# Optimization experiments

Hardware: AMD Instinct MI355X
Metric: run time of the kernel (lower is better)

Reference implementation:

```python
import jax, jax.numpy as jnp
import numpy as np

# ---- dimensions / config (match init_kwargs / RFM2DConfig defaults) ----
N = 128          # grid points per side
M = 128          # number of random features
B = 8            # batch of coefficient fields
H = 1.0 / (N - 1)
DT, ETA, STEPS = 0.03, 1e-4, 34          # heat-equation smoothing (eq. 3.14)
EPS, FVAL = 1e-9, 1.0
SP, SM, DSIG = 1.0 / 12.0, -1.0 / 3.0, 0.15  # sigma_gamma params (eq. 3.13)


def _dst1(x):
    """DST-I along last axis via odd-extension FFT (length 2*(n+1))."""
    n = x.shape[-1]
    z = jnp.zeros(x.shape[:-1] + (1,), x.dtype)
    y = jnp.concatenate([z, x, z, -jnp.flip(x, axis=-1)], axis=-1)
    return -jnp.fft.fft(y, axis=-1)[..., 1:n + 1].imag


def _dst2(x):
    y = _dst1(x)
    return jnp.swapaxes(_dst1(jnp.swapaxes(y, -1, -2)), -1, -2)


def _idst2(x):
    # inverse DST-I is DST-I / (2*(n+1)) per axis
    n1, n2 = x.shape[-1], x.shape[-2]
    return _dst2(x) / (4.0 * (n1 + 1) * (n2 + 1))


def _poisson_denom():
    n = N - 2
    k = np.arange(1, n + 1)
    lam = 2.0 - 2.0 * np.cos(np.pi * k / (n + 1))
    return jnp.asarray((lam[:, None] + lam[None, :]) / H ** 2, jnp.float32)

DENOM = _poisson_denom()  # (N-2, N-2)


def poisson_solve(rhs):
    """Solve -Lap u = rhs on (0,1)^2, homogeneous Dirichlet BC. rhs: (...,N,N)."""
    ri = rhs[..., 1:-1, 1:-1]
    ui = _idst2(_dst2(ri) / DENOM)
    pad = [(0, 0)] * (rhs.ndim - 2) + [(1, 1), (1, 1)]
    return jnp.pad(ui, pad)  # zero boundary


def lap_neumann(u):
    """5-point Laplacian with replicate (homogeneous Neumann) padding."""
    pad = [(0, 0)] * (u.ndim - 2) + [(1, 1), (1, 1)]
    up = jnp.pad(u, pad, mode='edge')
    return (up[..., 2:, 1:-1] + up[..., :-2, 1:-1]
            + up[..., 1:-1, 2:] + up[..., 1:-1, :-2] - 4.0 * u) / H ** 2


def grad_central(u):
    """Centered FD gradient, one-sided at boundaries. Returns (du/dx, du/dy)."""
    dudx = jnp.concatenate([(u[..., 1:2, :] - u[..., 0:1, :]) / H,
                            (u[..., 2:, :] - u[..., :-2, :]) / (2.0 * H),
                            (u[..., -1:, :] - u[..., -2:-1, :]) / H], axis=-2)
    dudy = jnp.concatenate([(u[..., :, 1:2] - u[..., :, 0:1]) / H,
                            (u[..., :, 2:] - u[..., :, :-2]) / (2.0 * H),
                            (u[..., :, -1:] - u[..., :, -2:-1]) / H], axis=-1)
    return dudx, dudy


def sigma_gamma(r):
    return (SP - SM) * jax.nn.sigmoid(r / DSIG) + SM


def smooth_coefficient(a):
    v = a
    for _ in range(STEPS):  # fixed small step count (34)
        v = v + DT * ETA * lap_neumann(v)
    return v


def setup_inputs() -> dict:
    key = jax.random.key(0)
    k1, k2, k3, k4 = jax.random.split(key, 4)
    # permeability field bounded away from 0 so log(a_eps) is well defined
    a = 1.0 + 2.0 * jax.random.uniform(k1, (B, N, N), dtype=jnp.float32)
    theta1 = jax.random.normal(k2, (M, N, N), dtype=jnp.float32)
    theta2 = jax.random.normal(k3, (M, N, N), dtype=jnp.float32)
    alpha = jax.random.normal(k4, (M,), dtype=jnp.float32)
    return {"a": a, "theta1": theta1, "theta2": theta2, "alpha": alpha}


def reference(a, theta1, theta2, alpha):
    # _prepare_a: heat-equation smoothing + grad(log a_eps)
    a_eps = smooth_coefficient(a)                       # (B,N,N)
    loga = jnp.log(jnp.maximum(a_eps, EPS))
    dlx, dly = grad_central(loga)                       # (B,N,N) each
    # predictor: -Lap p0 = f * sigma_gamma(theta1) / a_eps
    s1 = sigma_gamma(theta1)                            # (M,N,N)
    rhs0 = FVAL * s1[None] / a_eps[:, None]             # (B,M,N,N)
    p0 = poisson_solve(rhs0)
    # corrector: add grad(log a_eps) . grad(p0), modulated by sigma_gamma(theta2)
    g0x, g0y = grad_central(p0)
    s2 = sigma_gamma(theta2)
    rhs1 = rhs0 + (dlx[:, None] * g0x + dly[:, None] * g0y) * s2[None]
    phi = poisson_solve(rhs1)                           # (B,M,N,N) features
    # linear readout over features
    return jnp.einsum('m,bmxy->bxy', alpha, phi)
```

## Files before the change

kernel.cpp:

```cpp
#include <hip/hip_runtime.h>
#include <math.h>

#ifndef M_PI
#define M_PI 3.14159265358979323846
#endif

typedef unsigned short u16;
typedef __attribute__((ext_vector_type(8))) short bf16x8;
typedef __attribute__((ext_vector_type(4))) float f32x4;
typedef __attribute__((ext_vector_type(4), aligned(4))) float f32x4u;
typedef __attribute__((ext_vector_type(16))) float f32x16;

#define LDW 136
#define LDWF 132

__device__ __forceinline__ float sigma_gamma(float r) {
    float s = 1.0f / (1.0f + __expf(r * (-1.0f / 0.15f)));
    return 0.4166666666666667f * s - 0.3333333333333333f;
}

__device__ __forceinline__ void split1(float x, u16& h, u16& l) {
    unsigned u = __float_as_uint(x);
    unsigned hb = u & 0xffff0000u;
    h = (u16)(hb >> 16);
    float d = x - __uint_as_float(hb);
    unsigned ud = __float_as_uint(d);
    l = (u16)((ud + 0x7fffu + ((ud >> 16) & 1u)) >> 16);
}

__global__ __launch_bounds__(256) void k_prep(
    u16* __restrict__ Shi, u16* __restrict__ Slo,
    u16* __restrict__ Qhi, u16* __restrict__ Qlo,
    u16* __restrict__ QThi, u16* __restrict__ QTlo,
    float* __restrict__ DINV, float* __restrict__ G) {
    int id = blockIdx.x * 256 + threadIdx.x;
    if (id >= 16384) return;
    int r = id >> 7, c = id & 127;
    u16 h, l;
    float s = 0.f, di = 0.f;
    if (r < 126 && c < 126) {
        int prod = ((r + 1) * (c + 1)) % 254;
        s = (float)sin((double)prod * (M_PI / 127.0));
        double sr = sin((double)(r + 1) * (M_PI / 254.0));
        double sc = sin((double)(c + 1) * (M_PI / 254.0));
        di = (float)(16.0 / (64516.0 * 16129.0 * 4.0 * (sr * sr + sc * sc)));
    }
    split1(s, h, l); Shi[id] = h; Slo[id] = l;
    DINV[id] = di;
    double nc = (c == 0) ? sqrt(1.0 / 128.0) : sqrt(2.0 / 128.0);
    float q = (float)(nc * cos(M_PI * (double)c * (double)(2 * r + 1) / 256.0));
    split1(q, h, l); Qhi[id] = h; Qlo[id] = l;
    double nr = (r == 0) ? sqrt(1.0 / 128.0) : sqrt(2.0 / 128.0);
    float qt = (float)(nr * cos(M_PI * (double)r * (double)(2 * c + 1) / 256.0));
    split1(qt, h, l); QThi[id] = h; QTlo[id] = l;
    double lr = 2.0 * cos(M_PI * (double)r / 128.0) - 2.0;
    double lc = 2.0 * cos(M_PI * (double)c / 128.0) - 2.0;
    G[id] = (float)pow(1.0 + 0.03 * 1e-4 * 16129.0 * (lr + lc), 34.0);
}

__global__ __launch_bounds__(256) void k_sg(
    const float* __restrict__ th1, const float* __restrict__ th2,
    const float* __restrict__ alpha,
    float* __restrict__ SG1, float* __restrict__ SG2a) {
    int id = (blockIdx.x * 256 + threadIdx.x) * 4;
    int m = id >> 14;
    float al = alpha[m];
    f32x4 a = *(const f32x4*)(th1 + id);
    f32x4 b = *(const f32x4*)(th2 + id);
    f32x4 o1, o2;
#pragma unroll
    for (int j = 0; j < 4; ++j) {
        o1[j] = sigma_gamma(a[j]);
        o2[j] = al * sigma_gamma(b[j]);
    }
    *(f32x4*)(SG1 + id) = o1;
    *(f32x4*)(SG2a + id) = o2;
}

template <bool DOD, bool LAST>
__device__ __forceinline__ void mm_pass32(u16* Xhi, u16* Xlo, float* UF,
                                          const u16* WH, const u16* WL,
                                          const float* Dg, int rt, int ct,
                                          int l31, int hb) {
    const int colX = ct * 32 + l31;
    f32x4 dpre[4];
    if (DOD) {
#pragma unroll
        for (int g = 0; g < 4; ++g)
            dpre[g] = *(const f32x4*)(Dg + colX * 128 + rt * 32 + 8 * g + 4 * hb);
    }
    f32x16 acc;
#pragma unroll
    for (int i = 0; i < 16; ++i) acc[i] = 0.f;
    const u16* xh = Xhi + (rt * 32 + l31) * LDW + hb * 8;
    const u16* xl = Xlo + (rt * 32 + l31) * LDW + hb * 8;
    const u16* wh = WH + (ct * 32 + l31) * LDW + hb * 8;
    const u16* wl = WL + (ct * 32 + l31) * LDW + hb * 8;
#pragma unroll
    for (int s = 0; s < 8; ++s) {
        bf16x8 ah = *(const bf16x8*)(xh + s * 16);
        bf16x8 al = *(const bf16x8*)(xl + s * 16);
        bf16x8 bh = *(const bf16x8*)(wh + s * 16);
        bf16x8 bl = *(const bf16x8*)(wl + s * 16);
        acc = __builtin_amdgcn_mfma_f32_32x32x16_bf16(ah, bh, acc, 0, 0, 0);
        acc = __builtin_amdgcn_mfma_f32_32x32x16_bf16(al, bh, acc, 0, 0, 0);
        acc = __builtin_amdgcn_mfma_f32_32x32x16_bf16(ah, bl, acc, 0, 0, 0);
    }
    f32x4 o[4];
    uint2 uh[4], ul[4];
#pragma unroll
    for (int g = 0; g < 4; ++g) {
        float v0 = acc[4 * g], v1 = acc[4 * g + 1];
        float v2 = acc[4 * g + 2], v3 = acc[4 * g + 3];
        if (DOD) {
            v0 *= dpre[g][0]; v1 *= dpre[g][1];
            v2 *= dpre[g][2]; v3 *= dpre[g][3];
        }
        if (LAST) {
            o[g] = f32x4{v0, v1, v2, v3};
        } else {
            u16 h0, l0, h1, l1, h2, l2, h3, l3;
            split1(v0, h0, l0); split1(v1, h1, l1);
            split1(v2, h2, l2); split1(v3, h3, l3);
            uh[g].x = (unsigned)h0 | ((unsigned)h1 << 16);
            uh[g].y = (unsigned)h2 | ((unsigned)h3 << 16);
            ul[g].x = (unsigned)l0 | ((unsigned)l1 << 16);
            ul[g].y = (unsigned)l2 | ((unsigned)l3 << 16);
        }
    }
    __syncthreads();
#pragma unroll
    for (int g = 0; g < 4; ++g) {
        const int rbase = rt * 32 + 8 * g + 4 * hb;
        if (LAST) {
            *(f32x4*)(UF + colX * LDWF + rbase) = o[g];
        } else {
            *(uint2*)(Xhi + colX * LDW + rbase) = uh[g];
            *(uint2*)(Xlo + colX * LDW + rbase) = ul[g];
        }
    }
    __syncthreads();
}

template <int MODE>
__global__ __launch_bounds__(1024, 4) void k_mega(
    const u16* __restrict__ WHg, const u16* __restrict__ WLg,
    const u16* __restrict__ WHg2, const u16* __restrict__ WLg2,
    const float* __restrict__ Dmat,
    const float* __restrict__ src, const float* __restrict__ aux,
    const float* __restrict__ th2, const float* __restrict__ alpha,
    const float* __restrict__ dlxc, const float* __restrict__ dlyc,
    float* __restrict__ o1, float* __restrict__ o2, float* __restrict__ o3,
    float* __restrict__ o4) {
    __shared__ __align__(16) char SM[139264];
    u16* Xhi = (u16*)SM;
    u16* Xlo = (u16*)(SM + 34816);
    float* UF = (float*)SM;
    u16* WH = (u16*)(SM + 69632);
    u16* WL = (u16*)(SM + 104448);
    float* LG = (float*)(SM + 69632);

    const int tid = threadIdx.x;

    if (MODE == 0 && blockIdx.x >= 8) {
        float* red = (float*)SM;
        const int px0 = (blockIdx.x - 8) * 128;
        const int pl = tid & 127, mg = tid >> 7;
        float acc = 0.f;
        for (int i = 0; i < 16; ++i) {
            int m = mg * 16 + i;
            acc += alpha[m] * th2[m * 16384 + px0 + pl];
        }
        red[tid] = acc;
        __syncthreads();
        if (tid < 128) {
            float sum = 0.f;
#pragma unroll
            for (int g = 0; g < 8; ++g) sum += red[tid + g * 128];
            o4[px0 + tid] = sum;
        }
        return;
    }

    const int wave = tid >> 6, lane = tid & 63;
    const int rt = wave >> 2, ct = wave & 3;
    const int l31 = lane & 31, hb = lane >> 5;

    int b, m0;
    if (MODE == 1) { b = blockIdx.x >> 5; m0 = (blockIdx.x & 31) * 4; }
    else { b = blockIdx.x; m0 = 0; }

#pragma unroll
    for (int p = 0; p < 2; ++p) {
        int ch = tid + p * 1024;
        int r = ch >> 4, j0 = (ch & 15) * 8;
        *(uint4*)&WH[r * LDW + j0] = *(const uint4*)(WHg + r * 128 + j0);
        *(uint4*)&WL[r * LDW + j0] = *(const uint4*)(WLg + r * 128 + j0);
    }

    float tac[16];
    if (MODE == 1) {
#pragma unroll
        for (int i = 0; i < 16; ++i) tac[i] = 0.f;
    }

    const int ML = (MODE == 1) ? 4 : 1;
    for (int mi = 0; mi < ML; ++mi) {
#pragma unroll
        for (int p = 0; p < 2; ++p) {
            int ch = tid + p * 1024;
            int row = ch >> 4, c0 = (ch & 15) * 8;
            float v[8];
            if (MODE == 1) {
                const float* t1 = src + (size_t)(m0 + mi) * 16384;
                const float* iv = aux + b * 16384;
                if (row < 126) {
                    int base = (row + 1) * 128 + 1 + c0;
                    f32x4u ta = *(const f32x4u*)(t1 + base);
                    f32x4u tb = *(const f32x4u*)(t1 + base + 4);
                    f32x4u ia = *(const f32x4u*)(iv + base);
                    f32x4u ib = *(const f32x4u*)(iv + base + 4);
#pragma unroll
                    for (int j = 0; j < 8; ++j) {
                        float tv = (j < 4) ? ta[j] : tb[j - 4];
                        float ivv = (j < 4) ? ia[j] : ib[j - 4];
                        v[j] = (c0 + j < 126) ? tv * ivv : 0.f;
                    }
                } else {
#pragma unroll
                    for (int j = 0; j < 8; ++j) v[j] = 0.f;
                }
            } else {
                f32x4 p0 = *(const f32x4*)(src + b * 16384 + ch * 8);
                f32x4 p1 = *(const f32x4*)(src + b * 16384 + ch * 8 + 4);
#pragma unroll
                for (int j = 0; j < 4; ++j) { v[j] = p0[j]; v[j + 4] = p1[j]; }
            }
            unsigned hw[4], lw[4];
#pragma unroll
            for (int k = 0; k < 4; ++k) {
                u16 ha, la, hbb, lb;
                split1(v[2 * k], ha, la);
                split1(v[2 * k + 1], hbb, lb);
                hw[k] = (unsigned)ha | ((unsigned)hbb << 16);
                lw[k] = (unsigned)la | ((unsigned)lb << 16);
            }
            *(uint4*)&Xhi[row * LDW + c0] = make_uint4(hw[0], hw[1], hw[2], hw[3]);
            *(uint4*)&Xlo[row * LDW + c0] = make_uint4(lw[0], lw[1], lw[2], lw[3]);
        }
        __syncthreads();

        mm_pass32<false, false>(Xhi, Xlo, UF, WH, WL, nullptr, rt, ct, l31, hb);
        mm_pass32<true, false>(Xhi, Xlo, UF, WH, WL, Dmat, rt, ct, l31, hb);
        if (MODE == 0) {
#pragma unroll
            for (int p = 0; p < 2; ++p) {
                int ch = tid + p * 1024;
                int r = ch >> 4, j0 = (ch & 15) * 8;
                *(uint4*)&WH[r * LDW + j0] = *(const uint4*)(WHg2 + r * 128 + j0);
                *(uint4*)&WL[r * LDW + j0] = *(const uint4*)(WLg2 + r * 128 + j0);
            }
            __syncthreads();
        }
        mm_pass32<false, false>(Xhi, Xlo, UF, WH, WL, nullptr, rt, ct, l31, hb);
        mm_pass32<false, true>(Xhi, Xlo, UF, WH, WL, nullptr, rt, ct, l31, hb);

        if (MODE == 0) {
#pragma unroll
            for (int p = 0; p < 2; ++p) {
                int ch = tid + p * 1024;
                int row = ch >> 4, c0 = (ch & 15) * 8;
                f32x4 a0 = *(const f32x4*)(UF + row * LDWF + c0);
                f32x4 a1 = *(const f32x4*)(UF + row * LDWF + c0 + 4);
                f32x4 i0, i1, g0, g1;
#pragma unroll
                for (int j = 0; j < 4; ++j) {
                    i0[j] = 1.0f / a0[j]; i1[j] = 1.0f / a1[j];
                    g0[j] = logf(fmaxf(a0[j], 1e-9f));
                    g1[j] = logf(fmaxf(a1[j], 1e-9f));
                }
                *(f32x4*)(o1 + b * 16384 + ch * 8) = i0;
                *(f32x4*)(o1 + b * 16384 + ch * 8 + 4) = i1;
                *(f32x4*)(LG + row * LDWF + c0) = g0;
                *(f32x4*)(LG + row * LDWF + c0 + 4) = g1;
            }
            __syncthreads();
#pragma unroll
            for (int p = 0; p < 2; ++p) {
                int ch = tid + p * 1024;
                int i = ch >> 4, c0 = (ch & 15) * 8;
                if (i < 1 || i > 126) continue;
                f32x4 up0 = *(const f32x4*)(LG + (i + 1) * LDWF + c0);
                f32x4 up1 = *(const f32x4*)(LG + (i + 1) * LDWF + c0 + 4);
                f32x4 um0 = *(const f32x4*)(LG + (i - 1) * LDWF + c0);
                f32x4 um1 = *(const f32x4*)(LG + (i - 1) * LDWF + c0 + 4);
                float win[13];
                win[0] = (c0 > 0) ? LG[i * LDWF + c0 - 1] : 0.f;
                f32x4 va = *(const f32x4*)(LG + i * LDWF + c0);
                f32x4 vb = *(const f32x4*)(LG + i * LDWF + c0 + 4);
                f32x4 vc = *(const f32x4*)(LG + i * LDWF + c0 + 8);
#pragma unroll
                for (int j = 0; j < 4; ++j) {
                    win[1 + j] = va[j]; win[5 + j] = vb[j]; win[9 + j] = vc[j];
                }
#pragma unroll
                for (int e = 0; e < 8; ++e) {
                    int j = c0 + e;
                    if (j < 1 || j > 126) continue;
                    float upv = (e < 4) ? up0[e] : up1[e - 4];
                    float umv = (e < 4) ? um0[e] : um1[e - 4];
                    o2[b * 16384 + i * 128 + j] = 63.5f * (upv - umv);
                    o3[b * 16384 + i * 128 + j] = 63.5f * (win[e + 2] - win[e]);
                }
            }
        } else if (MODE == 1) {
            const float* t2 = th2 + (size_t)(m0 + mi) * 16384;
            const float* dxb = dlxc + b * 16384;
            const float* dyb = dlyc + b * 16384;
#pragma unroll
            for (int p = 0; p < 2; ++p) {
                int ch = tid + p * 1024;
                int i = ch >> 4, c0 = (ch & 15) * 8;
                if (i >= 126) continue;
                const int fbase = (i + 1) * 128 + c0 + 1;
                f32x4u t2a = *(const f32x4u*)(t2 + fbase);
                f32x4u t2b = *(const f32x4u*)(t2 + fbase + 4);
                f32x4u dxa = *(const f32x4u*)(dxb + fbase);
                f32x4u dxbv = *(const f32x4u*)(dxb + fbase + 4);
                f32x4u dya = *(const f32x4u*)(dyb + fbase);
                f32x4u dybv = *(const f32x4u*)(dyb + fbase + 4);
                f32x4 up0 = *(const f32x4*)(UF + (i + 1) * LDWF + c0);
                f32x4 up1 = *(const f32x4*)(UF + (i + 1) * LDWF + c0 + 4);
                f32x4 um0, um1;
                if (i > 0) {
                    um0 = *(const f32x4*)(UF + (i - 1) * LDWF + c0);
                    um1 = *(const f32x4*)(UF + (i - 1) * LDWF + c0 + 4);
                } else {
                    um0 = f32x4{0.f, 0.f, 0.f, 0.f}; um1 = um0;
                }
                float win[13];
                win[0] = (c0 > 0) ? UF[i * LDWF + c0 - 1] : 0.f;
                f32x4 va = *(const f32x4*)(UF + i * LDWF + c0);
                f32x4 vb = *(const f32x4*)(UF + i * LDWF + c0 + 4);
                f32x4 vc = *(const f32x4*)(UF + i * LDWF + c0 + 8);
#pragma unroll
                for (int j = 0; j < 4; ++j) {
                    win[1 + j] = va[j]; win[5 + j] = vb[j]; win[9 + j] = vc[j];
                }
#pragma unroll
                for (int e = 0; e < 8; ++e) {
                    int j = c0 + e;
                    if (j >= 126) continue;
                    float upv = (e < 4) ? up0[e] : up1[e - 4];
                    float umv = (e < 4) ? um0[e] : um1[e - 4];
                    float g0x = 63.5f * (upv - umv);
                    float g0y = 63.5f * (win[e + 2] - win[e]);
                    float s2a = (e < 4) ? t2a[e] : t2b[e - 4];
                    float dxv = (e < 4) ? dxa[e] : dxbv[e - 4];
                    float dyv = (e < 4) ? dya[e] : dybv[e - 4];
                    tac[p * 8 + e] += s2a * (dxv * g0x + dyv * g0y);
                }
            }
            __syncthreads();
        } else {
#pragma unroll
            for (int p = 0; p < 2; ++p) {
                int ch = tid + p * 1024;
                int r = ch >> 4, c0 = (ch & 15) * 8;
#pragma unroll
                for (int e = 0; e < 8; ++e) {
                    int c = c0 + e;
                    float v = 0.f;
                    if (r >= 1 && r <= 126 && c >= 1 && c <= 126)
                        v = UF[(r - 1) * LDWF + (c - 1)];
                    o1[b * 16384 + r * 128 + c] = v;
                }
            }
        }
    }
    if (MODE == 1) {
#pragma unroll
        for (int p = 0; p < 2; ++p) {
            int ch = tid + p * 1024;
            f32x4 w0 = {tac[p * 8], tac[p * 8 + 1], tac[p * 8 + 2], tac[p * 8 + 3]};
            f32x4 w1 = {tac[p * 8 + 4], tac[p * 8 + 5], tac[p * 8 + 6], tac[p * 8 + 7]};
            *(f32x4*)(o1 + (size_t)blockIdx.x * 16384 + ch * 8) = w0;
            *(f32x4*)(o1 + (size_t)blockIdx.x * 16384 + ch * 8 + 4) = w1;
        }
    }
}

__global__ __launch_bounds__(256) void k_reduce(const float* __restrict__ Pp,
                                                const float* __restrict__ inva,
                                                const float* __restrict__ S1a,
                                                float* __restrict__ R2) {
    int id = blockIdx.x * 256 + threadIdx.x;
    int b = id >> 12;
    int k = (id & 4095) * 4;
    int r = k >> 7, c0 = k & 127;
    f32x4 v = {0.f, 0.f, 0.f, 0.f};
    if (r < 126) {
        const float* tp = Pp + (size_t)(b * 32) * 16384 + k;
#pragma unroll 4
        for (int g = 0; g < 32; ++g) {
            f32x4 t = *(const f32x4*)(tp + (size_t)g * 16384);
            v.x += t.x; v.y += t.y; v.z += t.z; v.w += t.w;
        }
        int fi = (r + 1) * 128 + c0 + 1;
        const float* ivb = inva + b * 16384;
#pragma unroll
        for (int e = 0; e < 4; ++e) {
            int c = c0 + e;
            v[e] = (c < 126) ? (v[e] + ivb[fi + e] * S1a[fi + e]) : 0.f;
        }
    }
    *(f32x4*)(R2 + (size_t)id * 4) = v;
}

extern "C" void kernel_launch(void* const* d_in, const int* in_sizes, int n_in,
                              void* d_out, int out_size, void* d_ws,
                              size_t ws_size, hipStream_t stream) {
    const float* a      = (const float*)d_in[0];
    const float* theta1 = (const float*)d_in[1];
    const float* theta2 = (const float*)d_in[2];
    const float* alpha  = (const float*)d_in[3];
    float* out = (float*)d_out;

    float* w = (float*)d_ws;
    float* DINV = w;
    float* G    = w + 16384;
    float* inva = w + 32768;
    float* dlx  = w + 163840;
    float* dly  = w + 294912;
    float* S1a  = w + 425984;
    float* R2   = w + 442368;
    float* Pp   = w + 573440;
    u16* Shi  = (u16*)(w + 4767744);
    u16* Slo  = (u16*)(w + 4775936);
    u16* Qhi  = (u16*)(w + 4784128);
    u16* Qlo  = (u16*)(w + 4792320);
    u16* QThi = (u16*)(w + 4800512);
    u16* QTlo = (u16*)(w + 4808704);
    float* SG1  = w + 4816896;
    float* SG2a = w + 6914048;

    k_prep<<<64, 256, 0, stream>>>(Shi, Slo, Qhi, Qlo, QThi, QTlo, DINV, G);
    k_sg<<<2048, 256, 0, stream>>>(theta1, theta2, alpha, SG1, SG2a);

    k_mega<0><<<136, 1024, 0, stream>>>(QThi, QTlo, Qhi, Qlo, G, a, nullptr,
                                        SG1, alpha, nullptr, nullptr,
                                        inva, dlx, dly, S1a);

    k_mega<1><<<256, 1024, 0, stream>>>(Shi, Slo, nullptr, nullptr, DINV,
                                        SG1, inva, SG2a, alpha, dlx, dly,
                                        Pp, nullptr, nullptr, nullptr);

    k_reduce<<<128, 256, 0, stream>>>(Pp, inva, S1a, R2);

    k_mega<2><<<8, 1024, 0, stream>>>(Shi, Slo, nullptr, nullptr, DINV,
                                      R2, nullptr, nullptr, nullptr, nullptr,
                                      nullptr, out, nullptr, nullptr, nullptr);
}
```

Before: 124.2 us.

## Stream DST high-part operand from global in MFMA layout, shrink LDS, fuse prep kernels

Adds a pre-swizzled copy of the DST matrix's bf16 high part stored in the MFMA fragment order. In modes 1 and 2 the MFMA B-high operand is read directly from global/L2 instead of LDS, which drops the WH staging and cuts the shared-memory footprint from 139 KB to 104 KB, possibly allowing more resident blocks or less LDS traffic. The two setup kernels (constant prep and sigma_gamma) are merged into one launch. The cost is extra global-load latency inside the MFMA inner loop.

```diff
diff --git a/kernel.cpp b/kernel.cpp
--- a/kernel.cpp
+++ b/kernel.cpp
@@ -28,58 +28,74 @@
     l = (u16)((ud + 0x7fffu + ((ud >> 16) & 1u)) >> 16);
 }
 
-__global__ __launch_bounds__(256) void k_prep(
+__global__ __launch_bounds__(256) void k_prep_all(
     u16* __restrict__ Shi, u16* __restrict__ Slo,
     u16* __restrict__ Qhi, u16* __restrict__ Qlo,
     u16* __restrict__ QThi, u16* __restrict__ QTlo,
-    float* __restrict__ DINV, float* __restrict__ G) {
-    int id = blockIdx.x * 256 + threadIdx.x;
-    if (id >= 16384) return;
-    int r = id >> 7, c = id & 127;
-    u16 h, l;
-    float s = 0.f, di = 0.f;
-    if (r < 126 && c < 126) {
-        int prod = ((r + 1) * (c + 1)) % 254;
-        s = (float)sin((double)prod * (M_PI / 127.0));
-        double sr = sin((double)(r + 1) * (M_PI / 254.0));
-        double sc = sin((double)(c + 1) * (M_PI / 254.0));
-        di = (float)(16.0 / (64516.0 * 16129.0 * 4.0 * (sr * sr + sc * sc)));
-    }
-    split1(s, h, l); Shi[id] = h; Slo[id] = l;
-    DINV[id] = di;
-    double nc = (c == 0) ? sqrt(1.0 / 128.0) : sqrt(2.0 / 128.0);
-    float q = (float)(nc * cos(M_PI * (double)c * (double)(2 * r + 1) / 256.0));
-    split1(q, h, l); Qhi[id] = h; Qlo[id] = l;
-    double nr = (r == 0) ? sqrt(1.0 / 128.0) : sqrt(2.0 / 128.0);
-    float qt = (float)(nr * cos(M_PI * (double)r * (double)(2 * c + 1) / 256.0));
-    split1(qt, h, l); QThi[id] = h; QTlo[id] = l;
-    double lr = 2.0 * cos(M_PI * (double)r / 128.0) - 2.0;
-    double lc = 2.0 * cos(M_PI * (double)c / 128.0) - 2.0;
-    G[id] = (float)pow(1.0 + 0.03 * 1e-4 * 16129.0 * (lr + lc), 34.0);
-}
-
-__global__ __launch_bounds__(256) void k_sg(
+    float* __restrict__ DINV, float* __restrict__ G,
+    u16* __restrict__ BSh,
     const float* __restrict__ th1, const float* __restrict__ th2,
     const float* __restrict__ alpha,
     float* __restrict__ SG1, float* __restrict__ SG2a) {
-    int id = (blockIdx.x * 256 + threadIdx.x) * 4;
-    int m = id >> 14;
-    float al = alpha[m];
-    f32x4 a = *(const f32x4*)(th1 + id);
-    f32x4 b = *(const f32x4*)(th2 + id);
-    f32x4 o1, o2;
-#pragma unroll
-    for (int j = 0; j < 4; ++j) {
-        o1[j] = sigma_gamma(a[j]);
-        o2[j] = al * sigma_gamma(b[j]);
-    }
-    *(f32x4*)(SG1 + id) = o1;
-    *(f32x4*)(SG2a + id) = o2;
-}
-
-template <bool DOD, bool LAST>
+    const int blk = blockIdx.x;
+    if (blk < 64) {
+        int id = blk * 256 + threadIdx.x;
+        int r = id >> 7, c = id & 127;
+        u16 h, l;
+        float s = 0.f, di = 0.f;
+        if (r < 126 && c < 126) {
+            int prod = ((r + 1) * (c + 1)) % 254;
+            s = (float)sin((double)prod * (M_PI / 127.0));
+            double sr = sin((double)(r + 1) * (M_PI / 254.0));
+            double sc = sin((double)(c + 1) * (M_PI / 254.0));
+            di = (float)(16.0 / (64516.0 * 16129.0 * 4.0 * (sr * sr + sc * sc)));
+        }
+        split1(s, h, l); Shi[id] = h; Slo[id] = l;
+        DINV[id] = di;
+        double nc = (c == 0) ? sqrt(1.0 / 128.0) : sqrt(2.0 / 128.0);
+        float q = (float)(nc * cos(M_PI * (double)c * (double)(2 * r + 1) / 256.0));
+        split1(q, h, l); Qhi[id] = h; Qlo[id] = l;
+        double nr = (r == 0) ? sqrt(1.0 / 128.0) : sqrt(2.0 / 128.0);
+        float qt = (float)(nr * cos(M_PI * (double)r * (double)(2 * c + 1) / 256.0));
+        split1(qt, h, l); QThi[id] = h; QTlo[id] = l;
+        double lr = 2.0 * cos(M_PI * (double)r / 128.0) - 2.0;
+        double lc = 2.0 * cos(M_PI * (double)c / 128.0) - 2.0;
+        G[id] = (float)pow(1.0 + 0.03 * 1e-4 * 16129.0 * (lr + lc), 34.0);
+    } else if (blk < 128) {
+        int id = (blk - 64) * 256 + threadIdx.x;
+        int j = id & 7, chunk = id >> 3;
+        int col = chunk & 127, t = chunk >> 7;
+        int hb = t & 1, s = t >> 1;
+        int k = hb * 8 + s * 16 + j;
+        float v = 0.f;
+        if (col < 126 && k < 126) {
+            int prod = ((col + 1) * (k + 1)) % 254;
+            v = (float)sin((double)prod * (M_PI / 127.0));
+        }
+        u16 h, l;
+        split1(v, h, l);
+        BSh[id] = h;
+    } else {
+        int id = ((blk - 128) * 256 + threadIdx.x) * 4;
+        int m = id >> 14;
+        float al = alpha[m];
+        f32x4 a = *(const f32x4*)(th1 + id);
+        f32x4 b = *(const f32x4*)(th2 + id);
+        f32x4 o1, o2;
+#pragma unroll
+        for (int j = 0; j < 4; ++j) {
+            o1[j] = sigma_gamma(a[j]);
+            o2[j] = al * sigma_gamma(b[j]);
+        }
+        *(f32x4*)(SG1 + id) = o1;
+        *(f32x4*)(SG2a + id) = o2;
+    }
+}
+
+template <bool DOD, bool LAST, bool GB>
 __device__ __forceinline__ void mm_pass32(u16* Xhi, u16* Xlo, float* UF,
                                           const u16* WH, const u16* WL,
+                                          const u16* __restrict__ BSg,
                                           const float* Dg, int rt, int ct,
                                           int l31, int hb) {
     const int colX = ct * 32 + l31;
@@ -94,13 +110,15 @@
     for (int i = 0; i < 16; ++i) acc[i] = 0.f;
     const u16* xh = Xhi + (rt * 32 + l31) * LDW + hb * 8;
     const u16* xl = Xlo + (rt * 32 + l31) * LDW + hb * 8;
-    const u16* wh = WH + (ct * 32 + l31) * LDW + hb * 8;
+    const u16* wh = GB ? nullptr : (WH + (ct * 32 + l31) * LDW + hb * 8);
     const u16* wl = WL + (ct * 32 + l31) * LDW + hb * 8;
+    const u16* bsp = GB ? (BSg + hb * 1024 + colX * 8) : nullptr;
 #pragma unroll
     for (int s = 0; s < 8; ++s) {
         bf16x8 ah = *(const bf16x8*)(xh + s * 16);
         bf16x8 al = *(const bf16x8*)(xl + s * 16);
-        bf16x8 bh = *(const bf16x8*)(wh + s * 16);
+        bf16x8 bh = GB ? *(const bf16x8*)(bsp + s * 2048)
+                       : *(const bf16x8*)(wh + s * 16);
         bf16x8 bl = *(const bf16x8*)(wl + s * 16);
         acc = __builtin_amdgcn_mfma_f32_32x32x16_bf16(ah, bh, acc, 0, 0, 0);
         acc = __builtin_amdgcn_mfma_f32_32x32x16_bf16(al, bh, acc, 0, 0, 0);
@@ -146,18 +164,19 @@
 __global__ __launch_bounds__(1024, 4) void k_mega(
     const u16* __restrict__ WHg, const u16* __restrict__ WLg,
     const u16* __restrict__ WHg2, const u16* __restrict__ WLg2,
+    const u16* __restrict__ BSg,
     const float* __restrict__ Dmat,
     const float* __restrict__ src, const float* __restrict__ aux,
     const float* __restrict__ th2, const float* __restrict__ alpha,
     const float* __restrict__ dlxc, const float* __restrict__ dlyc,
     float* __restrict__ o1, float* __restrict__ o2, float* __restrict__ o3,
     float* __restrict__ o4) {
-    __shared__ __align__(16) char SM[139264];
+    __shared__ __align__(16) char SM[MODE == 0 ? 139264 : 104448];
     u16* Xhi = (u16*)SM;
     u16* Xlo = (u16*)(SM + 34816);
     float* UF = (float*)SM;
     u16* WH = (u16*)(SM + 69632);
-    u16* WL = (u16*)(SM + 104448);
+    u16* WL = (u16*)(MODE == 0 ? (SM + 104448) : (SM + 69632));
     float* LG = (float*)(SM + 69632);
 
     const int tid = threadIdx.x;
@@ -194,7 +213,8 @@
     for (int p = 0; p < 2; ++p) {
         int ch = tid + p * 1024;
         int r = ch >> 4, j0 = (ch & 15) * 8;
-        *(uint4*)&WH[r * LDW + j0] = *(const uint4*)(WHg + r * 128 + j0);
+        if (MODE == 0)
+            *(uint4*)&WH[r * LDW + j0] = *(const uint4*)(WHg + r * 128 + j0);
         *(uint4*)&WL[r * LDW + j0] = *(const uint4*)(WLg + r * 128 + j0);
     }
 
@@ -250,9 +270,9 @@
         }
         __syncthreads();
 
-        mm_pass32<false, false>(Xhi, Xlo, UF, WH, WL, nullptr, rt, ct, l31, hb);
-        mm_pass32<true, false>(Xhi, Xlo, UF, WH, WL, Dmat, rt, ct, l31, hb);
         if (MODE == 0) {
+            mm_pass32<false, false, false>(Xhi, Xlo, UF, WH, WL, nullptr, nullptr, rt, ct, l31, hb);
+            mm_pass32<true, false, false>(Xhi, Xlo, UF, WH, WL, nullptr, Dmat, rt, ct, l31, hb);
 #pragma unroll
             for (int p = 0; p < 2; ++p) {
                 int ch = tid + p * 1024;
@@ -261,9 +281,14 @@
                 *(uint4*)&WL[r * LDW + j0] = *(const uint4*)(WLg2 + r * 128 + j0);
             }
             __syncthreads();
-        }
-        mm_pass32<false, false>(Xhi, Xlo, UF, WH, WL, nullptr, rt, ct, l31, hb);
-        mm_pass32<false, true>(Xhi, Xlo, UF, WH, WL, nullptr, rt, ct, l31, hb);
+            mm_pass32<false, false, false>(Xhi, Xlo, UF, WH, WL, nullptr, nullptr, rt, ct, l31, hb);
+            mm_pass32<false, true, false>(Xhi, Xlo, UF, WH, WL, nullptr, nullptr, rt, ct, l31, hb);
+        } else {
+            mm_pass32<false, false, true>(Xhi, Xlo, UF, nullptr, WL, BSg, nullptr, rt, ct, l31, hb);
+            mm_pass32<true, false, true>(Xhi, Xlo, UF, nullptr, WL, BSg, Dmat, rt, ct, l31, hb);
+            mm_pass32<false, false, true>(Xhi, Xlo, UF, nullptr, WL, BSg, nullptr, rt, ct, l31, hb);
+            mm_pass32<false, true, true>(Xhi, Xlo, UF, nullptr, WL, BSg, nullptr, rt, ct, l31, hb);
+        }
 
         if (MODE == 0) {
 #pragma unroll
@@ -443,21 +468,24 @@
     u16* QTlo = (u16*)(w + 4808704);
     float* SG1  = w + 4816896;
     float* SG2a = w + 6914048;
-
-    k_prep<<<64, 256, 0, stream>>>(Shi, Slo, Qhi, Qlo, QThi, QTlo, DINV, G);
-    k_sg<<<2048, 256, 0, stream>>>(theta1, theta2, alpha, SG1, SG2a);
-
-    k_mega<0><<<136, 1024, 0, stream>>>(QThi, QTlo, Qhi, Qlo, G, a, nullptr,
-                                        SG1, alpha, nullptr, nullptr,
+    u16* BSh  = (u16*)(w + 9011200);
+
+    k_prep_all<<<2176, 256, 0, stream>>>(Shi, Slo, Qhi, Qlo, QThi, QTlo,
+                                         DINV, G, BSh, theta1, theta2, alpha,
+                                         SG1, SG2a);
+
+    k_mega<0><<<136, 1024, 0, stream>>>(QThi, QTlo, Qhi, Qlo, nullptr, G, a,
+                                        nullptr, SG1, alpha, nullptr, nullptr,
                                         inva, dlx, dly, S1a);
 
-    k_mega<1><<<256, 1024, 0, stream>>>(Shi, Slo, nullptr, nullptr, DINV,
-                                        SG1, inva, SG2a, alpha, dlx, dly,
+    k_mega<1><<<256, 1024, 0, stream>>>(nullptr, Slo, nullptr, nullptr, BSh,
+                                        DINV, SG1, inva, SG2a, alpha, dlx, dly,
                                         Pp, nullptr, nullptr, nullptr);
 
     k_reduce<<<128, 256, 0, stream>>>(Pp, inva, S1a, R2);
 
-    k_mega<2><<<8, 1024, 0, stream>>>(Shi, Slo, nullptr, nullptr, DINV,
-                                      R2, nullptr, nullptr, nullptr, nullptr,
-                                      nullptr, out, nullptr, nullptr, nullptr);
-}
+    k_mega<2><<<8, 1024, 0, stream>>>(nullptr, Slo, nullptr, nullptr, BSh,
+                                      DINV, R2, nullptr, nullptr, nullptr,
+                                      nullptr, nullptr, out, nullptr, nullptr,
+                                      nullptr);
+}
```

New measurement: 151.3 us. 1.22x slower.
